# Optimization experiments

Hardware: AMD Instinct MI355X
Metric: run time of the kernel (lower is better)

The kernel has to match this reference:

```python
import jax, jax.numpy as jnp
import numpy as np
from jax import lax

EPS = 1e-5


def _st_gcn_layer(x, w, b, A):
    # x: (N, C, T, V); w: (K*Co, C, 9, 1); A: (K, V, V) (already scaled by edge importance)
    y = lax.conv_general_dilated(x, w, window_strides=(1, 1),
                                 padding=[(4, 4), (0, 0)],
                                 dimension_numbers=('NCHW', 'OIHW', 'NCHW'))
    y = y + b[None, :, None, None]
    N, KC, T, V = y.shape
    K = A.shape[0]
    y = y.reshape(N, K, KC // K, T, V)
    y = jnp.einsum('nkctv,kvw->nctw', y, A)  # graph convolution
    return jax.nn.relu(y)


def setup_inputs() -> dict:
    key = jax.random.key(0)
    ks = jax.random.split(key, 8)
    N, T, V, C, Co, K, KT = 16, 512, 25, 256, 256, 3, 9
    x = jax.random.normal(ks[0], (N, T, V, C), dtype=jnp.float32)
    bn_gamma = jax.random.uniform(ks[1], (V * C,), dtype=jnp.float32)
    bn_beta = jax.random.normal(ks[2], (V * C,), dtype=jnp.float32)
    bn_mean = jnp.zeros((V * C,), dtype=jnp.float32)
    bn_var = jnp.ones((V * C,), dtype=jnp.float32)
    w_scale = 1.0 / np.sqrt(C * KT)
    w1 = jax.random.normal(ks[3], (K * Co, C, KT, 1), dtype=jnp.float32) * w_scale
    b1 = jax.random.normal(ks[4], (K * Co,), dtype=jnp.float32) * 0.01
    w2 = jax.random.normal(ks[5], (K * Co, Co, KT, 1), dtype=jnp.float32) * w_scale
    b2 = jax.random.normal(ks[6], (K * Co,), dtype=jnp.float32) * 0.01
    ei1 = jnp.ones((K, V, V), dtype=jnp.float32)
    ei2 = jnp.ones((K, V, V), dtype=jnp.float32)
    A = jax.random.uniform(ks[7], (K, V, V), dtype=jnp.float32)
    return {"x": x, "bn_gamma": bn_gamma, "bn_beta": bn_beta, "bn_mean": bn_mean,
            "bn_var": bn_var, "w1": w1, "b1": b1, "ei1": ei1, "w2": w2, "b2": b2,
            "ei2": ei2, "A": A}


def reference(x, bn_gamma, bn_beta, bn_mean, bn_var, w1, b1, ei1, w2, b2, ei2, A):
    N, T, V, C = x.shape
    # data_bn over V*C channels (V-major, C-minor per the torch permutes), eval mode
    xb = jnp.transpose(x, (0, 2, 3, 1)).reshape(N, V * C, T)  # (N, V*C, T)
    inv = bn_gamma / jnp.sqrt(bn_var + EPS)
    xb = (xb - bn_mean[None, :, None]) * inv[None, :, None] + bn_beta[None, :, None]
    xb = jnp.transpose(xb.reshape(N, V, C, T), (0, 2, 3, 1))  # (N, C, T, V)
    h = _st_gcn_layer(xb, w1, b1, A * ei1)
    h = _st_gcn_layer(h, w2, b2, A * ei2)
    return jnp.transpose(h, (0, 2, 3, 1))  # (N, T, V, Cout)
```

## Files before the change

kernel.cpp:

```cpp
#include <hip/hip_runtime.h>
#include <stdint.h>

typedef unsigned short ushortT;
typedef short short8 __attribute__((ext_vector_type(8)));
typedef float f32x4 __attribute__((ext_vector_type(4)));
typedef float f32x2 __attribute__((ext_vector_type(2)));
typedef unsigned short us4 __attribute__((ext_vector_type(4)));

#define TP 520
#define PAD 4
#define XTILE_B (264 * 64)
#define ATILE_B (128 * 64)
#define APAIR_B (2 * ATILE_B)

__device__ __forceinline__ unsigned short f2bf(float f) {
  union { float f; unsigned int u; } v; v.f = f;
  unsigned int r = (v.u + 0x7fffu + ((v.u >> 16) & 1u)) >> 16;
  return (unsigned short)r;
}
__device__ __forceinline__ float bf2f(unsigned short b) {
  union { unsigned int u; float f; } v; v.u = ((unsigned int)b) << 16;
  return v.f;
}
__device__ __forceinline__ float ldadp(const void* p, long i, int bf) {
  return bf ? bf2f(((const unsigned short*)p)[i]) : ((const float*)p)[i];
}
__device__ __forceinline__ f32x2 ldadp2(const void* p, long i, int bf) {
  f32x2 r;
  if (bf) {
    unsigned int u = *(const unsigned int*)((const unsigned short*)p + i);
    r[0] = bf2f((unsigned short)(u & 0xffffu));
    r[1] = bf2f((unsigned short)(u >> 16));
  } else {
    r = *(const f32x2*)((const float*)p + i);
  }
  return r;
}

__device__ __forceinline__ void gload16(const void* g, void* l) {
  __builtin_amdgcn_global_load_lds(
      (const __attribute__((address_space(1))) void*)g,
      (__attribute__((address_space(3))) void*)l, 16, 0, 0);
}

__global__ void detect_kernel(const void* var, int* flags) {
  flags[0] = (((const unsigned int*)var)[0] == 0x3F803F80u) ? 1 : 0;
}

__global__ void prep_w_kernel(const void* w, ushortT* __restrict__ Wt, const int* flags) {
  int bf = flags[0];
  long i = (long)blockIdx.x * 256 + threadIdx.x;
  int c = (int)(i & 255);
  long mc = i >> 8;
  int m = (int)(mc % 768);
  int dt = (int)(mc / 768);
  long dst = (((long)(dt * 8 + (c >> 5)) * 768 + m) << 5) + (c & 31);
  Wt[dst] = f2bf(ldadp(w, ((long)m * 256 + c) * 9 + dt, bf));
}

__global__ void prep_ae_kernel(const void* A, const void* ei, const void* b,
                               float* __restrict__ Ae, float* __restrict__ Bsum,
                               const int* flags) {
  __shared__ float ash[1875];
  int bf = flags[0];
  int tid = threadIdx.x;
  for (int i = tid; i < 1875; i += 1024) {
    float ae = ldadp(A, i, bf) * ldadp(ei, i, bf);
    ash[i] = ae; Ae[i] = ae;
  }
  __syncthreads();
  for (int i = tid; i < 6400; i += 1024) {
    int c = i / 25, w = i % 25;
    float s = 0.f;
    for (int k = 0; k < 3; k++) {
      float cs = 0.f;
      for (int v = 0; v < 25; v++) cs += ash[(k * 25 + v) * 25 + w];
      s += ldadp(b, k * 256 + c, bf) * cs;
    }
    Bsum[i] = s;
  }
}

__global__ void pad_kernel(ushortT* __restrict__ Xb) {
  long nv = (long)blockIdx.y * 25 + blockIdx.x;
  int tid = threadIdx.x;
  #pragma unroll
  for (int r = 0; r < 4; r++) {
    Xb[(nv * TP + r) * 256 + tid] = 0;
    Xb[(nv * TP + 516 + r) * 256 + tid] = 0;
  }
}

__global__ void bn_kernel(const void* x, long xoff, const void* gamma, const void* beta,
                          const void* mean, const void* var, const int* flags,
                          ushortT* __restrict__ Xb, long total) {
  long i2 = ((long)blockIdx.x * 256 + threadIdx.x) * 2;
  if (i2 >= total) return;
  int bf = flags[0];
  int c = (int)(i2 & 255);
  long j = i2 >> 8;
  int v = (int)(j % 25); j /= 25;
  int t = (int)(j % 512); j /= 512;
  int nl = (int)j;
  int pc = v * 256 + c;
  f32x2 xv = ldadp2(x, xoff + i2, bf);
  unsigned int outw = 0;
  #pragma unroll
  for (int e = 0; e < 2; e++) {
    float inv = ldadp(gamma, pc + e, bf) * rsqrtf(ldadp(var, pc + e, bf) + 1e-5f);
    float val = (xv[e] - ldadp(mean, pc + e, bf)) * inv + ldadp(beta, pc + e, bf);
    outw |= ((unsigned int)f2bf(val)) << (16 * e);
  }
  *(unsigned int*)(Xb + (((long)(nl * 25 + v)) * TP + t + PAD) * 256 + c) = outw;
}

__global__ __launch_bounds__(256, 2) void conv_kernel(
    const ushortT* __restrict__ Xb, const ushortT* __restrict__ Wt,
    ushortT* __restrict__ Y) {
  __shared__ short8 smem[(2 * XTILE_B + 2 * APAIR_B) / 16];
  char* lds = (char*)smem;
  char* Xl[2] = { lds, lds + XTILE_B };
  char* Ap[2] = { lds + 2 * XTILE_B, lds + 2 * XTILE_B + APAIR_B };

  const int tid = threadIdx.x;
  const int lane = tid & 63;
  const int wave = tid >> 6;
  const int wm = wave >> 1, wn = wave & 1;
  const int kb = lane >> 4;
  const int l15 = lane & 15;
  const int wubase = (tid & ~63);

  int bid = blockIdx.x;
  const int v = bid % 25;
  const int rtile = bid / 25;
  const int tt = rtile & 1;
  const int mt = rtile >> 1;
  const int nl = blockIdx.y;
  const int m0 = mt * 128;
  const int t0 = tt * 256;

  const long xrowbase = ((long)(nl * 25 + v)) * TP + t0;

  auto stageX = [&](int cc, char* xb) {
    #pragma unroll
    for (int k = 0; k < 4; k++) {
      int s = k * 256 + tid;
      int r = s >> 2, q = s & 3;
      int ql = q ^ ((r >> 1) & 3);
      gload16(Xb + (xrowbase + r) * 256 + cc * 32 + ql * 8,
              xb + (long)(k * 256 + wubase) * 16);
    }
    if (tid < 32) {
      int s = 1024 + tid;
      int r = s >> 2, q = s & 3;
      int ql = q ^ ((r >> 1) & 3);
      gload16(Xb + (xrowbase + r) * 256 + cc * 32 + ql * 8,
              xb + (long)1024 * 16);
    }
  };
  auto stageA = [&](int cc, int dt0, int cnt, char* ab) {
    for (int d = 0; d < cnt; d++) {
      const ushortT* wb = Wt + (((long)((dt0 + d) * 8 + cc) * 768 + m0) << 5);
      #pragma unroll
      for (int k = 0; k < 2; k++) {
        int s = k * 256 + tid;
        int r = s >> 2, q = s & 3;
        int ql = q ^ ((r >> 1) & 3);
        gload16(wb + (long)(r * 4 + ql) * 8,
                ab + (long)d * ATILE_B + (long)(k * 256 + wubase) * 16);
      }
    }
  };

  f32x4 acc[4][8];
  #pragma unroll
  for (int i = 0; i < 4; i++)
    #pragma unroll
    for (int j = 0; j < 8; j++) { acc[i][j][0]=0.f; acc[i][j][1]=0.f; acc[i][j][2]=0.f; acc[i][j][3]=0.f; }

  stageX(0, Xl[0]);
  stageA(0, 0, 2, Ap[0]);
  __syncthreads();

  for (int cc = 0; cc < 8; cc++) {
    char* Xcur = Xl[cc & 1];
    for (int sub = 0; sub < 5; sub++) {
      const int p = cc * 5 + sub;
      if (sub == 0 && cc < 7) stageX(cc + 1, Xl[(cc + 1) & 1]);
      if (p < 39) {
        int np = p + 1;
        int ncc = np / 5, nsub = np % 5;
        stageA(ncc, (nsub < 4) ? 2 * nsub : 8, (nsub < 4) ? 2 : 1, Ap[np & 1]);
      }

      const char* Acur = Ap[p & 1];
      const int ndt = (sub < 4) ? 2 : 1;
      for (int d = 0; d < ndt; d++) {
        const int dt = 2 * sub + d;
        short8 a[4], b[8];
        #pragma unroll
        for (int i = 0; i < 4; i++) {
          int r = wm * 64 + i * 16 + l15;
          int sl = kb ^ ((r >> 1) & 3);
          a[i] = *(const short8*)(Acur + d * ATILE_B + r * 64 + sl * 16);
        }
        #pragma unroll
        for (int j = 0; j < 8; j++) {
          int r = wn * 128 + j * 16 + l15 + dt;
          int sl = kb ^ ((r >> 1) & 3);
          b[j] = *(const short8*)(Xcur + r * 64 + sl * 16);
        }
        #pragma unroll
        for (int i = 0; i < 4; i++)
          #pragma unroll
          for (int j = 0; j < 8; j++)
            acc[i][j] = __builtin_amdgcn_mfma_f32_16x16x32_bf16(a[i], b[j], acc[i][j], 0, 0, 0);
      }
      __syncthreads();
    }
  }

  #pragma unroll
  for (int i = 0; i < 4; i++) {
    #pragma unroll
    for (int j = 0; j < 8; j++) {
      int tg = t0 + wn * 128 + j * 16 + l15;
      int kc = m0 + wm * 64 + i * 16 + (kb << 2);
      long off = (((long)(nl * 512 + tg)) * 25 + v) * 768 + kc;
      us4 u;
      u[0] = f2bf(acc[i][j][0]);
      u[1] = f2bf(acc[i][j][1]);
      u[2] = f2bf(acc[i][j][2]);
      u[3] = f2bf(acc[i][j][3]);
      *(us4*)(Y + off) = u;
    }
  }
}

__global__ __launch_bounds__(256) void gconv_kernel(
    const ushortT* __restrict__ Y, const float* __restrict__ Ae,
    const float* __restrict__ Bsum, ushortT* __restrict__ dstb,
    float* __restrict__ dstf, int mode) {
  __shared__ float aesh[1875];
  const int tid = threadIdx.x;
  const int cp = tid & 127;
  const int c  = cp * 2;
  const int th = tid >> 7;
  const int nl = blockIdx.y;
  const int t0 = blockIdx.x << 2;
  const int tA = t0 + 2 * th;
  for (int i = tid; i < 1875; i += 256) aesh[i] = Ae[i];
  __syncthreads();

  float acc[2][2][25];
  #pragma unroll
  for (int w = 0; w < 25; w++) {
    float b0 = Bsum[c * 25 + w], b1 = Bsum[(c + 1) * 25 + w];
    acc[0][0][w] = b0; acc[0][1][w] = b0;
    acc[1][0][w] = b1; acc[1][1][w] = b1;
  }
  for (int k = 0; k < 3; k++) {
    for (int v = 0; v < 25; v++) {
      long ybase = (((long)(nl * 512 + tA)) * 25 + v) * 768 + k * 256 + c;
      unsigned int ua = *(const unsigned int*)(Y + ybase);
      unsigned int ub = *(const unsigned int*)(Y + ybase + 25L * 768);
      float ya0 = bf2f((unsigned short)(ua & 0xffffu));
      float ya1 = bf2f((unsigned short)(ua >> 16));
      float yb0 = bf2f((unsigned short)(ub & 0xffffu));
      float yb1 = bf2f((unsigned short)(ub >> 16));
      const float* ap = &aesh[(k * 25 + v) * 25];
      #pragma unroll
      for (int w = 0; w < 25; w++) {
        float a = ap[w];
        acc[0][0][w] = fmaf(ya0, a, acc[0][0][w]);
        acc[1][0][w] = fmaf(ya1, a, acc[1][0][w]);
        acc[0][1][w] = fmaf(yb0, a, acc[0][1][w]);
        acc[1][1][w] = fmaf(yb1, a, acc[1][1][w]);
      }
    }
  }
  #pragma unroll
  for (int tt = 0; tt < 2; tt++) {
    int t = tA + tt;
    #pragma unroll
    for (int w = 0; w < 25; w++) {
      float v0 = acc[0][tt][w]; v0 = v0 > 0.f ? v0 : 0.f;
      float v1 = acc[1][tt][w]; v1 = v1 > 0.f ? v1 : 0.f;
      if (mode == 0) {
        unsigned int pk = (unsigned int)f2bf(v0) | ((unsigned int)f2bf(v1) << 16);
        *(unsigned int*)(dstb + (((long)(nl * 25 + w)) * TP + t + PAD) * 256 + c) = pk;
      } else {
        f32x2 pk; pk[0] = v0; pk[1] = v1;
        *(f32x2*)(dstf + (((long)(nl * 512 + t)) * 25 + w) * 256 + c) = pk;
      }
    }
  }
}

extern "C" void kernel_launch(void* const* d_in, const int* in_sizes, int n_in,
                              void* d_out, int out_size, void* d_ws, size_t ws_size,
                              hipStream_t stream) {
  const void* x     = d_in[0];
  const void* gamma = d_in[1];
  const void* beta  = d_in[2];
  const void* mean  = d_in[3];
  const void* var   = d_in[4];
  const void* w1    = d_in[5];
  const void* b1    = d_in[6];
  const void* ei1   = d_in[7];
  const void* w2    = d_in[8];
  const void* b2    = d_in[9];
  const void* ei2   = d_in[10];
  const void* A     = d_in[11];
  float* out = (float*)d_out;

  const size_t WtB  = 9L * 768 * 256 * 2;
  const size_t XbB1 = 25L * TP * 256 * 2;
  const size_t YB1  = 512L * 25 * 768 * 2;
  const size_t fixed = 256 + 2 * WtB + 2 * (1875 * 4) + 2 * (6400 * 4) + 8 * 256;

  int G = 16;
  while (G > 1 && fixed + (size_t)G * (XbB1 + YB1) > ws_size) G >>= 1;

  char* ws = (char*)d_ws;
  size_t off = 0;
  auto alloc = [&](size_t bytes) { char* p = ws + off; off = (off + bytes + 255) & ~(size_t)255; return p; };
  int* flags   = (int*)alloc(256);
  ushortT* Wt1 = (ushortT*)alloc(WtB);
  ushortT* Wt2 = (ushortT*)alloc(WtB);
  float* Ae1   = (float*)alloc(1875 * 4);
  float* Ae2   = (float*)alloc(1875 * 4);
  float* Bs1   = (float*)alloc(6400 * 4);
  float* Bs2   = (float*)alloc(6400 * 4);
  ushortT* Xb  = (ushortT*)alloc((size_t)G * XbB1);
  ushortT* Y   = (ushortT*)alloc((size_t)G * YB1);

  detect_kernel<<<1, 1, 0, stream>>>(var, flags);
  prep_w_kernel<<<6912, 256, 0, stream>>>(w1, Wt1, flags);
  prep_w_kernel<<<6912, 256, 0, stream>>>(w2, Wt2, flags);
  prep_ae_kernel<<<1, 1024, 0, stream>>>(A, ei1, b1, Ae1, Bs1, flags);
  prep_ae_kernel<<<1, 1024, 0, stream>>>(A, ei2, b2, Ae2, Bs2, flags);

  for (int n0 = 0; n0 < 16; n0 += G) {
    long xoff = (long)n0 * 512 * 25 * 256;
    float* out_c = out + (size_t)n0 * 512 * 25 * 256;
    long total = (long)G * 512 * 25 * 256;

    pad_kernel<<<dim3(25, G), 256, 0, stream>>>(Xb);
    bn_kernel<<<(int)((total / 2 + 255) / 256), 256, 0, stream>>>(x, xoff, gamma, beta, mean, var, flags, Xb, total);

    conv_kernel<<<dim3(300, G), 256, 0, stream>>>(Xb, Wt1, Y);
    gconv_kernel<<<dim3(128, G), 256, 0, stream>>>(Y, Ae1, Bs1, Xb, (float*)nullptr, 0);
    conv_kernel<<<dim3(300, G), 256, 0, stream>>>(Xb, Wt2, Y);
    gconv_kernel<<<dim3(128, G), 256, 0, stream>>>(Y, Ae2, Bs2, (ushortT*)nullptr, out_c, 1);
  }
}
```

Measured before the change: 2.021 ms.

## Triple-buffer weight tiles with fine-grained vmcnt waits and one barrier per tap

Restructures the conv kernel's main loop so each of the 9 temporal taps gets its own weight tile. The tiles go into a three-slot ring buffer and are prefetched two taps ahead. Full __syncthreads are replaced by explicit s_waitcnt vmcnt counts plus a raw s_barrier, so outstanding global-to-LDS loads can overlap compute. The X tile load is made uniform across five iterations with a clamped tail row. The counted waits depend on an exact ordering of load issues, so any miscount risks races. LDS use changes slightly, which may affect the two-blocks-per-CU occupancy.

```diff
diff --git a/kernel.cpp b/kernel.cpp
--- a/kernel.cpp
+++ b/kernel.cpp
@@ -9,9 +9,8 @@
 
 #define TP 520
 #define PAD 4
-#define XTILE_B (264 * 64)
-#define ATILE_B (128 * 64)
-#define APAIR_B (2 * ATILE_B)
+#define XPAD_B 20480
+#define ATILE_B 8192
 
 __device__ __forceinline__ unsigned short f2bf(float f) {
   union { float f; unsigned int u; } v; v.f = f;
@@ -117,10 +116,13 @@
 __global__ __launch_bounds__(256, 2) void conv_kernel(
     const ushortT* __restrict__ Xb, const ushortT* __restrict__ Wt,
     ushortT* __restrict__ Y) {
-  __shared__ short8 smem[(2 * XTILE_B + 2 * APAIR_B) / 16];
+  __shared__ short8 smem[(2 * XPAD_B + 3 * ATILE_B) / 16];
   char* lds = (char*)smem;
-  char* Xl[2] = { lds, lds + XTILE_B };
-  char* Ap[2] = { lds + 2 * XTILE_B, lds + 2 * XTILE_B + APAIR_B };
+  char* Xl0 = lds;
+  char* Xl1 = lds + XPAD_B;
+  char* Ap0 = lds + 2 * XPAD_B;
+  char* Ap1 = Ap0 + ATILE_B;
+  char* Ap2 = Ap0 + 2 * ATILE_B;
 
   const int tid = threadIdx.x;
   const int lane = tid & 63;
@@ -143,80 +145,73 @@
 
   auto stageX = [&](int cc, char* xb) {
     #pragma unroll
-    for (int k = 0; k < 4; k++) {
+    for (int k = 0; k < 5; k++) {
+      int s = k * 256 + tid;
+      int r = s >> 2, q = s & 3;
+      if (k == 4) r = (r < 264) ? r : 263;
+      int ql = q ^ ((r >> 1) & 3);
+      gload16(Xb + (xrowbase + r) * 256 + cc * 32 + ql * 8,
+              xb + (long)(k * 256 + wubase) * 16);
+    }
+  };
+  auto stageA = [&](int g, char* ab) {
+    const ushortT* wb = Wt + (((long)g * 768 + m0) << 5);
+    #pragma unroll
+    for (int k = 0; k < 2; k++) {
       int s = k * 256 + tid;
       int r = s >> 2, q = s & 3;
       int ql = q ^ ((r >> 1) & 3);
-      gload16(Xb + (xrowbase + r) * 256 + cc * 32 + ql * 8,
-              xb + (long)(k * 256 + wubase) * 16);
-    }
-    if (tid < 32) {
-      int s = 1024 + tid;
-      int r = s >> 2, q = s & 3;
-      int ql = q ^ ((r >> 1) & 3);
-      gload16(Xb + (xrowbase + r) * 256 + cc * 32 + ql * 8,
-              xb + (long)1024 * 16);
+      gload16(wb + (long)(r * 4 + ql) * 8, ab + (long)(k * 256 + wubase) * 16);
     }
   };
-  auto stageA = [&](int cc, int dt0, int cnt, char* ab) {
-    for (int d = 0; d < cnt; d++) {
-      const ushortT* wb = Wt + (((long)((dt0 + d) * 8 + cc) * 768 + m0) << 5);
+
+  f32x4 acc[4][8];
+  #pragma unroll
+  for (int i = 0; i < 4; i++)
+    #pragma unroll
+    for (int j = 0; j < 8; j++) { acc[i][j][0]=0.f; acc[i][j][1]=0.f; acc[i][j][2]=0.f; acc[i][j][3]=0.f; }
+
+  stageX(0, Xl0);
+  stageA(0, Ap0);
+  stageA(8, Ap1);
+
+  for (int cc = 0; cc < 8; cc++) {
+    char* Xcur = (cc & 1) ? Xl1 : Xl0;
+    char* Xnext = (cc & 1) ? Xl0 : Xl1;
+    #pragma unroll
+    for (int dt = 0; dt < 9; dt++) {
+      if (dt == 8) { asm volatile("s_waitcnt vmcnt(7)" ::: "memory"); }
+      else         { asm volatile("s_waitcnt vmcnt(2)" ::: "memory"); }
+      __builtin_amdgcn_s_barrier();
+
+      if (dt <= 6) {
+        stageA((dt + 2) * 8 + cc, (dt + 2) % 3 == 0 ? Ap0 : ((dt + 2) % 3 == 1 ? Ap1 : Ap2));
+      } else if (dt == 7) {
+        stageA(cc + 1, Ap0);
+        stageX(cc + 1, Xnext);
+      } else {
+        stageA(8 + cc + 1, Ap1);
+      }
+
+      const char* Acur = (dt % 3 == 0) ? Ap0 : ((dt % 3 == 1) ? Ap1 : Ap2);
+      short8 a[4], b[8];
       #pragma unroll
-      for (int k = 0; k < 2; k++) {
-        int s = k * 256 + tid;
-        int r = s >> 2, q = s & 3;
-        int ql = q ^ ((r >> 1) & 3);
-        gload16(wb + (long)(r * 4 + ql) * 8,
-                ab + (long)d * ATILE_B + (long)(k * 256 + wubase) * 16);
-      }
-    }
-  };
-
-  f32x4 acc[4][8];
-  #pragma unroll
-  for (int i = 0; i < 4; i++)
-    #pragma unroll
-    for (int j = 0; j < 8; j++) { acc[i][j][0]=0.f; acc[i][j][1]=0.f; acc[i][j][2]=0.f; acc[i][j][3]=0.f; }
-
-  stageX(0, Xl[0]);
-  stageA(0, 0, 2, Ap[0]);
-  __syncthreads();
-
-  for (int cc = 0; cc < 8; cc++) {
-    char* Xcur = Xl[cc & 1];
-    for (int sub = 0; sub < 5; sub++) {
-      const int p = cc * 5 + sub;
-      if (sub == 0 && cc < 7) stageX(cc + 1, Xl[(cc + 1) & 1]);
-      if (p < 39) {
-        int np = p + 1;
-        int ncc = np / 5, nsub = np % 5;
-        stageA(ncc, (nsub < 4) ? 2 * nsub : 8, (nsub < 4) ? 2 : 1, Ap[np & 1]);
-      }
-
-      const char* Acur = Ap[p & 1];
-      const int ndt = (sub < 4) ? 2 : 1;
-      for (int d = 0; d < ndt; d++) {
-        const int dt = 2 * sub + d;
-        short8 a[4], b[8];
+      for (int i = 0; i < 4; i++) {
+        int r = wm * 64 + i * 16 + l15;
+        int sl = kb ^ ((r >> 1) & 3);
+        a[i] = *(const short8*)(Acur + r * 64 + sl * 16);
+      }
+      #pragma unroll
+      for (int j = 0; j < 8; j++) {
+        int r = wn * 128 + j * 16 + l15 + dt;
+        int sl = kb ^ ((r >> 1) & 3);
+        b[j] = *(const short8*)(Xcur + r * 64 + sl * 16);
+      }
+      #pragma unroll
+      for (int i = 0; i < 4; i++)
         #pragma unroll
-        for (int i = 0; i < 4; i++) {
-          int r = wm * 64 + i * 16 + l15;
-          int sl = kb ^ ((r >> 1) & 3);
-          a[i] = *(const short8*)(Acur + d * ATILE_B + r * 64 + sl * 16);
-        }
-        #pragma unroll
-        for (int j = 0; j < 8; j++) {
-          int r = wn * 128 + j * 16 + l15 + dt;
-          int sl = kb ^ ((r >> 1) & 3);
-          b[j] = *(const short8*)(Xcur + r * 64 + sl * 16);
-        }
-        #pragma unroll
-        for (int i = 0; i < 4; i++)
-          #pragma unroll
-          for (int j = 0; j < 8; j++)
-            acc[i][j] = __builtin_amdgcn_mfma_f32_16x16x32_bf16(a[i], b[j], acc[i][j], 0, 0, 0);
-      }
-      __syncthreads();
+        for (int j = 0; j < 8; j++)
+          acc[i][j] = __builtin_amdgcn_mfma_f32_16x16x32_bf16(a[i], b[j], acc[i][j], 0, 0, 0);
     }
   }
 
```

Result: faster. 1.694 ms (-16.2%).
